# Kernel tuning notes

Measured on AMD Instinct MI355X. Metric: run time of the kernel, lower is better.

## Reference

```python
import jax, jax.numpy as jnp
import numpy as np

B, N, D = 8, 900, 256
SA_H, CA_H = 8, 8
L, P = 4, 4
FF = 2048
SHAPES = ((128, 128), (64, 64), (32, 32), (16, 16))
STARTS = (0, 16384, 20480, 21504)
S = 21760
D_BAND = (D // 6) * 2   # 84
D_ROPE = 3 * D_BAND     # 252
NF = D_BAND // 2        # 42
EPS = 1e-5


def _ln(x, g, b):
    mu = jnp.mean(x, -1, keepdims=True)
    var = jnp.mean((x - mu) ** 2, -1, keepdims=True)
    return (x - mu) * jax.lax.rsqrt(var + EPS) * g + b


def _rotate_half(x):
    x1 = x[..., 0::2]
    x2 = x[..., 1::2]
    return jnp.stack([-x2, x1], axis=-1).reshape(x.shape)


def _rope(q, k, boxes):
    freqs = 1.0 / (10000.0 ** (jnp.arange(NF, dtype=jnp.float32) / NF))
    cx, cy = boxes[..., 0], boxes[..., 1]
    xy = cx * cy

    def cs(v, f):
        a = v[..., None] * f
        return jnp.repeat(jnp.cos(a), 2, -1), jnp.repeat(jnp.sin(a), 2, -1)

    cx_c, cx_s = cs(cx, freqs)
    cy_c, cy_s = cs(cy, freqs)
    xy_c, xy_s = cs(xy, freqs * 0.1)
    cos = jnp.concatenate([cx_c, cy_c, xy_c], -1)
    sin = jnp.concatenate([cx_s, cy_s, xy_s], -1)

    def app(t):
        a, rest = t[..., :D_ROPE], t[..., D_ROPE:]
        return jnp.concatenate([a * cos + _rotate_half(a) * sin, rest], -1)

    return app(q), app(k)


def _bilinear(img, xy):
    # img: (Hl, Wl, C); xy: (M, 2) normalized in [0,1]
    # torch grid_sample semantics: align_corners=False, zero padding
    Hl, Wl, _ = img.shape
    x = xy[:, 0] * Wl - 0.5
    y = xy[:, 1] * Hl - 0.5
    x0 = jnp.floor(x)
    y0 = jnp.floor(y)
    lx = x - x0
    ly = y - y0
    x0i = x0.astype(jnp.int32)
    y0i = y0.astype(jnp.int32)

    def tap(yi, xi):
        valid = (xi >= 0) & (xi < Wl) & (yi >= 0) & (yi < Hl)
        v = img[jnp.clip(yi, 0, Hl - 1), jnp.clip(xi, 0, Wl - 1)]
        return v * valid[:, None].astype(v.dtype)

    return (tap(y0i, x0i) * ((1 - ly) * (1 - lx))[:, None]
            + tap(y0i, x0i + 1) * ((1 - ly) * lx)[:, None]
            + tap(y0i + 1, x0i) * (ly * (1 - lx))[:, None]
            + tap(y0i + 1, x0i + 1) * (ly * lx)[:, None])


def _forward(tgt, memory, query_pos, ref_boxes, reference_points,
             wq, bq, wk, bk, wv, bv, sa_wo, sa_bo, n1_g, n1_b,
             off_w, off_b, aw_w, aw_b, val_w, val_b, co_w, co_b,
             n2_g, n2_b, ff1_w, ff1_b, ff2_w, ff2_b, n3_g, n3_b):
    dh = D // SA_H
    # --- self attention with ComplexRoPE2D applied pre-projection ---
    q = tgt + query_pos
    k = tgt + query_pos
    q, k = _rope(q, k, ref_boxes)
    qh = (q @ wq + bq).reshape(B, N, SA_H, dh).transpose(0, 2, 1, 3)
    kh = (k @ wk + bk).reshape(B, N, SA_H, dh).transpose(0, 2, 1, 3)
    vh = (tgt @ wv + bv).reshape(B, N, SA_H, dh).transpose(0, 2, 1, 3)
    att = jax.nn.softmax(jnp.einsum('bhqd,bhkd->bhqk', qh, kh) * (dh ** -0.5), axis=-1)
    sa = jnp.einsum('bhqk,bhkd->bhqd', att, vh).transpose(0, 2, 1, 3).reshape(B, N, D)
    tgt = _ln(tgt + sa @ sa_wo + sa_bo, n1_g, n1_b)

    # --- multi-scale deformable cross-attention ---
    cdh = D // CA_H
    q2 = tgt + query_pos
    value = (memory @ val_w + val_b).reshape(B, S, CA_H, cdh)
    off = (q2 @ off_w + off_b).reshape(B, N, CA_H, L, P, 2)
    aw = jax.nn.softmax((q2 @ aw_w + aw_b).reshape(B, N, CA_H, L * P), axis=-1)
    aw = aw.reshape(B, N, CA_H, L, P)
    # offset normalizer is (W, H) per level
    normalizer = jnp.array([[w_, h_] for (h_, w_) in SHAPES], dtype=jnp.float32)
    loc = reference_points[:, :, None, :, None, :] + off / normalizer[None, None, None, :, None, :]
    out = jnp.zeros((B, CA_H, N, cdh), dtype=tgt.dtype)
    for l, (Hl, Wl) in enumerate(SHAPES):
        st = STARTS[l]
        v_l = value[:, st:st + Hl * Wl].reshape(B, Hl, Wl, CA_H, cdh)
        v_l = v_l.transpose(0, 3, 1, 2, 4).reshape(B * CA_H, Hl, Wl, cdh)
        loc_l = loc[:, :, :, l].transpose(0, 2, 1, 3, 4).reshape(B * CA_H, N * P, 2)
        s_l = jax.vmap(_bilinear)(v_l, loc_l).reshape(B, CA_H, N, P, cdh)
        out = out + jnp.einsum('bhnpd,bnhp->bhnd', s_l, aw[:, :, :, l])
    ca = out.transpose(0, 2, 1, 3).reshape(B, N, D) @ co_w + co_b
    tgt = _ln(tgt + ca, n2_g, n2_b)

    # --- FFN ---
    ff = jax.nn.relu(tgt @ ff1_w + ff1_b) @ ff2_w + ff2_b
    return _ln(tgt + ff, n3_g, n3_b)


def setup_inputs() -> dict:
    key = jax.random.key(0)
    ks = jax.random.split(key, 16)

    def wmat(k, shape):
        return jax.random.normal(k, shape, jnp.float32) * 0.02

    z = lambda *s: jnp.zeros(s, jnp.float32)
    o = lambda *s: jnp.ones(s, jnp.float32)
    return dict(
        tgt=jax.random.normal(ks[0], (B, N, D), jnp.float32),
        memory=jax.random.normal(ks[1], (B, S, D), jnp.float32),
        query_pos=jax.random.normal(ks[2], (B, N, D), jnp.float32) * 0.02,
        ref_boxes=jax.random.uniform(ks[3], (B, N, 4), jnp.float32),
        reference_points=jax.random.uniform(ks[4], (B, N, L, 2), jnp.float32),
        wq=wmat(ks[5], (D, D)), bq=z(D),
        wk=wmat(ks[6], (D, D)), bk=z(D),
        wv=wmat(ks[7], (D, D)), bv=z(D),
        sa_wo=wmat(ks[8], (D, D)), sa_bo=z(D),
        n1_g=o(D), n1_b=z(D),
        off_w=wmat(ks[9], (D, CA_H * L * P * 2)), off_b=z(CA_H * L * P * 2),
        aw_w=wmat(ks[10], (D, CA_H * L * P)), aw_b=z(CA_H * L * P),
        val_w=wmat(ks[11], (D, D)), val_b=z(D),
        co_w=wmat(ks[12], (D, D)), co_b=z(D),
        n2_g=o(D), n2_b=z(D),
        ff1_w=wmat(ks[13], (D, FF)), ff1_b=z(FF),
        ff2_w=wmat(ks[14], (FF, D)), ff2_b=z(D),
        n3_g=o(D), n3_b=z(D))


def reference(tgt, memory, query_pos, ref_boxes, reference_points,
              wq, bq, wk, bk, wv, bv, sa_wo, sa_bo, n1_g, n1_b,
              off_w, off_b, aw_w, aw_b, val_w, val_b, co_w, co_b,
              n2_g, n2_b, ff1_w, ff1_b, ff2_w, ff2_b, n3_g, n3_b):
    return _forward(tgt, memory, query_pos, ref_boxes, reference_points,
                    wq, bq, wk, bk, wv, bv, sa_wo, sa_bo, n1_g, n1_b,
                    off_w, off_b, aw_w, aw_b, val_w, val_b, co_w, co_b,
                    n2_g, n2_b, ff1_w, ff1_b, ff2_w, ff2_b, n3_g, n3_b)
```

## Files before the change

### kernel.cpp

```cpp
#include <hip/hip_runtime.h>
#include <hip/hip_bf16.h>
#include <math.h>

#define B_ 8
#define N_ 900
#define D_ 256
#define S_ 21760
#define H_ 8
#define DH 32
#define FF_ 2048
#define NROWS (B_*N_)

typedef __attribute__((ext_vector_type(8))) short bf16x8;
typedef __attribute__((ext_vector_type(4))) float f32x4;

union BU { bf16x8 v; short s[8]; unsigned long long u[2]; };

static __device__ inline short f2bf_s(float x) {
  __hip_bfloat16 h = __float2bfloat16(x);
  return *reinterpret_cast<short*>(&h);
}

__device__ __forceinline__ void gload_lds16(const float* g, float* lds) {
  __builtin_amdgcn_global_load_lds(
      (const __attribute__((address_space(1))) void*)g,
      (__attribute__((address_space(3))) void*)lds, 16, 0, 0);
}

__global__ __launch_bounds__(128) void rope_kernel(
    const float* __restrict__ tgt, const float* __restrict__ qpos,
    const float* __restrict__ boxes, __hip_bfloat16* __restrict__ out)
{
  int row = blockIdx.x;
  int tid = threadIdx.x;
  const float* x = tgt  + (size_t)row * D_;
  const float* p = qpos + (size_t)row * D_;
  float a0 = x[2*tid]   + p[2*tid];
  float a1 = x[2*tid+1] + p[2*tid+1];
  float o0 = a0, o1 = a1;
  if (tid < 126) {
    int band = tid / 42;
    int fi   = tid - band * 42;
    float freq = powf(10000.0f, -(float)fi / 42.0f);
    float cx = boxes[(size_t)row*4 + 0];
    float cy = boxes[(size_t)row*4 + 1];
    float v  = (band == 0) ? cx : (band == 1 ? cy : cx * cy);
    if (band == 2) freq *= 0.1f;
    float ang = v * freq;
    float c = cosf(ang), s = sinf(ang);
    o0 = a0 * c - a1 * s;
    o1 = a1 * c + a0 * s;
  }
  short2 sv = make_short2(f2bf_s(o0), f2bf_s(o1));
  *(short2*)&out[(size_t)row*D_ + 2*tid] = sv;
}

__global__ __launch_bounds__(256) void wtrans_kernel(
    const float* __restrict__ wq, const float* __restrict__ wk,
    const float* __restrict__ wv, const float* __restrict__ sa_wo,
    const float* __restrict__ offw, const float* __restrict__ valw,
    const float* __restrict__ cow, const float* __restrict__ aww,
    const float* __restrict__ ff1w, const float* __restrict__ ff2w,
    short* __restrict__ Wt)
{
  int bid = blockIdx.x;
  const float* W; short* out; int K, N, tile;
  if (bid < 448) {
    int wi = bid >> 6; tile = bid & 63; K = 256; N = 256;
    const float* tab[7] = {wq, wk, wv, sa_wo, offw, valw, cow};
    const int   off[7]  = {0, 65536, 131072, 196608, 262144, 360448, 425984};
    W = tab[wi]; out = Wt + off[wi];
  } else if (bid < 480) {
    tile = bid - 448; K = 256; N = 128; W = aww; out = Wt + 327680;
  } else if (bid < 992) {
    tile = bid - 480; K = 256; N = 2048; W = ff1w; out = Wt + 491520;
  } else {
    tile = bid - 992; K = 2048; N = 256; W = ff2w; out = Wt + 1015808;
  }
  int ntn = N >> 5;
  int tk = tile / ntn, tn = tile - tk * ntn;
  __shared__ float t[32][33];
  int c = threadIdx.x & 31, rr = threadIdx.x >> 5;
  #pragma unroll
  for (int i = 0; i < 4; ++i)
    t[rr + i*8][c] = W[(size_t)(tk*32 + rr + i*8) * N + tn*32 + c];
  __syncthreads();
  #pragma unroll
  for (int i = 0; i < 4; ++i)
    out[(size_t)(tn*32 + rr + i*8) * K + tk*32 + c] = f2bf_s(t[c][rr + i*8]);
}

template<int BM, int KK, bool ABF16, bool A2ADD, bool RELU, int OUTMODE, int AUX>
__global__ __launch_bounds__(256) void mgemm_kernel(
    const void* __restrict__ Ap, const float* __restrict__ A2p,
    const short* __restrict__ Wt,
    const float* __restrict__ bias, const float* __restrict__ bias2,
    void* __restrict__ Cp, void* __restrict__ Cp2, int M, int N,
    const float* __restrict__ Xres, const float* __restrict__ lng,
    const float* __restrict__ lnb)
{
  constexpr int MS = BM / 16;
  constexpr bool SWAP = (OUTMODE != 2);
  __shared__ short As[BM * 256];
  int tid = threadIdx.x;
  int w = tid >> 6, lane = tid & 63;
  int g = lane >> 4, r = lane & 15;
  int m0 = blockIdx.x * BM;
  int nw = blockIdx.y * 256 + w * 64;
  bool active = nw < N;

  f32x4 acc[MS][4];
  #pragma unroll
  for (int i = 0; i < MS; ++i)
    #pragma unroll
    for (int j = 0; j < 4; ++j) acc[i][j] = (f32x4){0.f,0.f,0.f,0.f};

  for (int kb = 0; kb < KK; kb += 256) {
    if (KK > 256 && kb) __syncthreads();
    #pragma unroll
    for (int i = 0; i < BM/8; ++i) {
      int u = i*256 + tid;
      int row = u >> 5, c8 = u & 31;
      BU pk;
      if (ABF16) {
        pk.v = *(const bf16x8*)((const short*)Ap + (size_t)(m0+row)*KK + kb + c8*8);
      } else {
        const float* ap = (const float*)Ap + (size_t)(m0+row)*KK + kb + c8*8;
        float4 a0 = *(const float4*)ap;
        float4 a1 = *(const float4*)(ap + 4);
        if (A2ADD) {
          const float* a2 = A2p + (size_t)(m0+row)*KK + kb + c8*8;
          float4 b0 = *(const float4*)a2;
          float4 b1 = *(const float4*)(a2 + 4);
          a0.x += b0.x; a0.y += b0.y; a0.z += b0.z; a0.w += b0.w;
          a1.x += b1.x; a1.y += b1.y; a1.z += b1.z; a1.w += b1.w;
        }
        pk.s[0]=f2bf_s(a0.x); pk.s[1]=f2bf_s(a0.y); pk.s[2]=f2bf_s(a0.z); pk.s[3]=f2bf_s(a0.w);
        pk.s[4]=f2bf_s(a1.x); pk.s[5]=f2bf_s(a1.y); pk.s[6]=f2bf_s(a1.z); pk.s[7]=f2bf_s(a1.w);
      }
      int col = (c8*8) ^ ((row & 7) << 3);
      *(bf16x8*)&As[row*256 + col] = pk.v;
    }
    __syncthreads();
    if (active) {
      #pragma unroll
      for (int kk = 0; kk < 8; ++kk) {
        BU bfr[4];
        #pragma unroll
        for (int ns = 0; ns < 4; ++ns) {
          const short* wp = Wt + (size_t)(nw + ns*16 + r)*KK + kb + kk*32;
          bfr[ns].u[0] = *(const unsigned long long*)(wp + 4*g);
          bfr[ns].u[1] = *(const unsigned long long*)(wp + 16 + 4*g);
        }
        #pragma unroll
        for (int ms = 0; ms < MS; ++ms) {
          int row = ms*16 + r;
          int c0 = (kk*32 + g*4)      ^ ((r & 7) << 3);
          int c1 = (kk*32 + 16 + g*4) ^ ((r & 7) << 3);
          BU af;
          af.u[0] = *(const unsigned long long*)&As[row*256 + c0];
          af.u[1] = *(const unsigned long long*)&As[row*256 + c1];
          #pragma unroll
          for (int ns = 0; ns < 4; ++ns) {
            if (SWAP)
              acc[ms][ns] = __builtin_amdgcn_mfma_f32_16x16x32_bf16(
                  bfr[ns].v, af.v, acc[ms][ns], 0, 0, 0);
            else
              acc[ms][ns] = __builtin_amdgcn_mfma_f32_16x16x32_bf16(
                  af.v, bfr[ns].v, acc[ms][ns], 0, 0, 0);
          }
        }
      }
    }
  }

  if (OUTMODE == 5) {
    float vv[MS][16];
    float ps[MS], pq[MS];
    #pragma unroll
    for (int ms = 0; ms < MS; ++ms) {
      ps[ms] = 0.f; pq[ms] = 0.f;
      int m = m0 + ms*16 + r;
      #pragma unroll
      for (int ns = 0; ns < 4; ++ns) {
        int n0 = nw + ns*16 + g*4;
        float4 b4 = *(const float4*)&bias[n0];
        float4 x4 = *(const float4*)&Xres[(size_t)m*256 + n0];
        #pragma unroll
        for (int j = 0; j < 4; ++j) {
          float v = acc[ms][ns][j] + ((const float*)&b4)[j] + ((const float*)&x4)[j];
          vv[ms][ns*4 + j] = v;
          ps[ms] += v; pq[ms] += v*v;
        }
      }
      ps[ms] += __shfl_xor(ps[ms], 16); ps[ms] += __shfl_xor(ps[ms], 32);
      pq[ms] += __shfl_xor(pq[ms], 16); pq[ms] += __shfl_xor(pq[ms], 32);
    }
    __syncthreads();
    float* red = (float*)As;
    if (g == 0) {
      #pragma unroll
      for (int ms = 0; ms < MS; ++ms) {
        red[(ms*16 + r)*8 + w]     = ps[ms];
        red[(ms*16 + r)*8 + 4 + w] = pq[ms];
      }
    }
    __syncthreads();
    #pragma unroll
    for (int ms = 0; ms < MS; ++ms) {
      int rowi = ms*16 + r;
      float ts = red[rowi*8+0]+red[rowi*8+1]+red[rowi*8+2]+red[rowi*8+3];
      float tq = red[rowi*8+4]+red[rowi*8+5]+red[rowi*8+6]+red[rowi*8+7];
      float mu = ts * (1.0f/256.0f);
      float var = tq * (1.0f/256.0f) - mu*mu;
      float rs = rsqrtf(fmaxf(var, 0.f) + 1e-5f);
      int m = m0 + ms*16 + r;
      #pragma unroll
      for (int ns = 0; ns < 4; ++ns) {
        int n0 = nw + ns*16 + g*4;
        float4 g4 = *(const float4*)&lng[n0];
        float4 be = *(const float4*)&lnb[n0];
        float4 ov;
        ov.x = (vv[ms][ns*4+0] - mu)*rs*g4.x + be.x;
        ov.y = (vv[ms][ns*4+1] - mu)*rs*g4.y + be.y;
        ov.z = (vv[ms][ns*4+2] - mu)*rs*g4.z + be.z;
        ov.w = (vv[ms][ns*4+3] - mu)*rs*g4.w + be.w;
        *(float4*)&((float*)Cp)[(size_t)m*256 + n0] = ov;
        if (AUX == 1) {
          float4 q4 = *(const float4*)&A2p[(size_t)m*256 + n0];
          short4 sv = make_short4(
              f2bf_s(ov.x + q4.x), f2bf_s(ov.y + q4.y),
              f2bf_s(ov.z + q4.z), f2bf_s(ov.w + q4.w));
          *(short4*)&((short*)Cp2)[(size_t)m*256 + n0] = sv;
        } else if (AUX == 2) {
          short4 sv = make_short4(
              f2bf_s(ov.x), f2bf_s(ov.y), f2bf_s(ov.z), f2bf_s(ov.w));
          *(short4*)&((short*)Cp2)[(size_t)m*256 + n0] = sv;
        }
      }
    }
    return;
  }

  if (!active) return;

  #pragma unroll
  for (int ms = 0; ms < MS; ++ms) {
    #pragma unroll
    for (int ns = 0; ns < 4; ++ns) {
      if (SWAP) {
        int n0 = nw + ns*16 + g*4;
        int m  = m0 + ms*16 + r;
        float4 b4;
        if (OUTMODE == 3 || OUTMODE == 4)
          b4 = (n0 < 256) ? *(const float4*)&bias[n0]
                          : *(const float4*)&bias2[n0 - 256];
        else
          b4 = *(const float4*)&bias[n0];
        float v0 = acc[ms][ns][0] + b4.x;
        float v1 = acc[ms][ns][1] + b4.y;
        float v2 = acc[ms][ns][2] + b4.z;
        float v3 = acc[ms][ns][3] + b4.w;
        if (RELU) {
          v0 = fmaxf(v0, 0.f); v1 = fmaxf(v1, 0.f);
          v2 = fmaxf(v2, 0.f); v3 = fmaxf(v3, 0.f);
        }
        if (OUTMODE == 0) {
          *(float4*)&((float*)Cp)[(size_t)m*N + n0] = make_float4(v0,v1,v2,v3);
        } else if (OUTMODE == 1) {
          short4 sv = make_short4(f2bf_s(v0), f2bf_s(v1), f2bf_s(v2), f2bf_s(v3));
          *(short4*)&((short*)Cp)[(size_t)m*N + n0] = sv;
        } else if (OUTMODE == 3) {
          short4 sv = make_short4(f2bf_s(v0), f2bf_s(v1), f2bf_s(v2), f2bf_s(v3));
          if (n0 < 256) *(short4*)&((short*)Cp )[(size_t)m*256 + n0]       = sv;
          else          *(short4*)&((short*)Cp2)[(size_t)m*256 + (n0-256)] = sv;
        } else {
          float4 fv = make_float4(v0,v1,v2,v3);
          if (n0 < 256) *(float4*)&((float*)Cp )[(size_t)m*256 + n0]       = fv;
          else          *(float4*)&((float*)Cp2)[(size_t)m*128 + (n0-256)] = fv;
        }
      } else {
        int n = nw + ns*16 + r;
        float bsc = bias[n];
        int hh = n >> 5, dd = n & 31;
        int mb = m0 + ms*16 + g*4;
        short4 sv = make_short4(
            f2bf_s(acc[ms][ns][0] + bsc), f2bf_s(acc[ms][ns][1] + bsc),
            f2bf_s(acc[ms][ns][2] + bsc), f2bf_s(acc[ms][ns][3] + bsc));
        int bb = mb / N_, bbe = (mb + 3) / N_;
        if (bb == bbe) {
          int nn = mb - bb * N_;
          *(short4*)&((short*)Cp)[((size_t)((bb*H_ + hh)*DH + dd))*N_ + nn] = sv;
        } else {
          const short* sp = (const short*)&sv;
          #pragma unroll
          for (int j = 0; j < 4; ++j) {
            int m = mb + j;
            int b2 = m / N_, nn = m - b2 * N_;
            ((short*)Cp)[((size_t)((b2*H_ + hh)*DH + dd))*N_ + nn] = sp[j];
          }
        }
      }
    }
  }
}

__global__ __launch_bounds__(512) void vgemm_kernel(
    const float* __restrict__ Ap, const short* __restrict__ Wt,
    const float* __restrict__ bias, short* __restrict__ Cp)
{
  __shared__ float buf[8][1024];
  __shared__ float dump[1024];
  int tid = threadIdx.x;
  int w = tid >> 6, l = tid & 63;
  int g = l >> 4, r = l & 15;
  int nw = w * 32;

  BU wreg[2][8];
  #pragma unroll
  for (int ns = 0; ns < 2; ++ns) {
    const short* wp = Wt + (size_t)(nw + ns*16 + r) * 256;
    #pragma unroll
    for (int kk = 0; kk < 8; ++kk) {
      wreg[ns][kk].u[0] = *(const unsigned long long*)(wp + kk*32 + 4*g);
      wreg[ns][kk].u[1] = *(const unsigned long long*)(wp + kk*32 + 16 + 4*g);
    }
  }
  float4 bs4[2];
  #pragma unroll
  for (int ns = 0; ns < 2; ++ns) bs4[ns] = *(const float4*)&bias[nw + ns*16 + g*4];

  bool stager = (w < 4);
  int srow = (w & 3)*8 + (l >> 3);
  int schunk = (l & 7) ^ (srow & 7);
  const float* gbase = Ap + ((size_t)blockIdx.x*160 + srow) * 256 + schunk*4;

  if (stager) {
    #pragma unroll
    for (int t = 0; t < 4; ++t)
      gload_lds16(gbase + (t>>3)*8192 + (t&7)*32, &buf[t][(w & 3)*256]);
  }

  f32x4 acc[2][2];
  #pragma unroll
  for (int i = 0; i < 2; ++i)
    #pragma unroll
    for (int j = 0; j < 2; ++j) acc[i][j] = (f32x4){0.f,0.f,0.f,0.f};

  int bb = blockIdx.x / 136;
  int pixblk = (blockIdx.x % 136) * 160;

  for (int s = 0; s < 5; ++s) {
    #pragma unroll
    for (int cp = 0; cp < 4; ++cp) {
      int c = cp*2;
      int t = s*8 + c;
      if (stager) {
        int tn0 = t + 4, tn1 = t + 5;
        if (tn0 < 40) gload_lds16(gbase + (tn0>>3)*8192 + (tn0&7)*32,
                                  &buf[(c+4)&7][(w & 3)*256]);
        else          gload_lds16(gbase, &dump[(w & 3)*256]);
        if (tn1 < 40) gload_lds16(gbase + (tn1>>3)*8192 + (tn1&7)*32,
                                  &buf[(c+5)&7][(w & 3)*256]);
        else          gload_lds16(gbase, &dump[(w & 3)*256]);
        asm volatile("s_waitcnt vmcnt(4)" ::: "memory");
      }
      __builtin_amdgcn_s_barrier();
      #pragma unroll
      for (int cc = 0; cc < 2; ++cc) {
        int ci = c + cc;
        const float* bp = &buf[ci][0];
        #pragma unroll
        for (int ms = 0; ms < 2; ++ms) {
          int row = ms*16 + r;
          const float* rp = bp + row*32;
          float4 f0 = *(const float4*)&rp[((g    ) ^ (row & 7)) * 4];
          float4 f1 = *(const float4*)&rp[((g + 4) ^ (row & 7)) * 4];
          BU af;
          af.s[0]=f2bf_s(f0.x); af.s[1]=f2bf_s(f0.y); af.s[2]=f2bf_s(f0.z); af.s[3]=f2bf_s(f0.w);
          af.s[4]=f2bf_s(f1.x); af.s[5]=f2bf_s(f1.y); af.s[6]=f2bf_s(f1.z); af.s[7]=f2bf_s(f1.w);
          #pragma unroll
          for (int ns = 0; ns < 2; ++ns)
            acc[ms][ns] = __builtin_amdgcn_mfma_f32_16x16x32_bf16(
                wreg[ns][ci].v, af.v, acc[ms][ns], 0, 0, 0);
        }
      }
    }
    int pix0 = pixblk + s*32;
    #pragma unroll
    for (int ms = 0; ms < 2; ++ms) {
      #pragma unroll
      for (int ns = 0; ns < 2; ++ns) {
        int pix = pix0 + ms*16 + r;
        int n0  = nw + ns*16 + g*4;
        int hh = n0 >> 5, dd = n0 & 31;
        short4 sv = make_short4(
            f2bf_s(acc[ms][ns][0] + bs4[ns].x),
            f2bf_s(acc[ms][ns][1] + bs4[ns].y),
            f2bf_s(acc[ms][ns][2] + bs4[ns].z),
            f2bf_s(acc[ms][ns][3] + bs4[ns].w));
        *(short4*)&Cp[((size_t)(bb*H_ + hh)*S_ + pix)*32 + dd] = sv;
        acc[ms][ns] = (f32x4){0.f,0.f,0.f,0.f};
      }
    }
  }
}

__global__ __launch_bounds__(64) void mfma_attn_kernel(
    const __hip_bfloat16* __restrict__ Q,
    const __hip_bfloat16* __restrict__ K,
    const __hip_bfloat16* __restrict__ Vt,
    __hip_bfloat16* __restrict__ O)
{
  const int NQT = 29;
  int wid = blockIdx.x;
  int qt = wid % NQT, bh = wid / NQT;
  int b = bh >> 3, h = bh & 7;
  int lane = threadIdx.x;
  int g = lane >> 4, r = lane & 15;
  int q0 = qt * 32;
  const float scale = 0.17677669529663687f;

  union U { bf16x8 v; short s[8]; unsigned long long u64[2]; };

  U qf[2];
  #pragma unroll
  for (int qq = 0; qq < 2; ++qq) {
    int qrow = min(q0 + qq*16 + r, N_ - 1);
    const __hip_bfloat16* qp = Q + ((size_t)(b*N_ + qrow))*D_ + h*DH;
    qf[qq].u64[0] = *(const unsigned long long*)(qp + 4*g);
    qf[qq].u64[1] = *(const unsigned long long*)(qp + 16 + 4*g);
  }

  f32x4 oaccA[2], oaccB[2];
  #pragma unroll
  for (int qq = 0; qq < 2; ++qq) {
    oaccA[qq] = (f32x4){0.f,0.f,0.f,0.f};
    oaccB[qq] = (f32x4){0.f,0.f,0.f,0.f};
  }
  float m0v = -1e30f, m1v = -1e30f, l0v = 0.f, l1v = 0.f;
  const f32x4 zero = {0.f,0.f,0.f,0.f};

  const __hip_bfloat16* vbase0 = Vt + (size_t)(bh*DH + r) * N_;
  const __hip_bfloat16* vbase1 = Vt + (size_t)(bh*DH + 16 + r) * N_;

  for (int kt = 0; kt < N_; kt += 32) {
    U kf0, kf1;
    {
      int kr0 = min(kt + r, N_ - 1);
      int kr1 = min(kt + 16 + r, N_ - 1);
      const __hip_bfloat16* kp0 = K + ((size_t)(b*N_ + kr0))*D_ + h*DH;
      const __hip_bfloat16* kp1 = K + ((size_t)(b*N_ + kr1))*D_ + h*DH;
      kf0.u64[0] = *(const unsigned long long*)(kp0 + 4*g);
      kf0.u64[1] = *(const unsigned long long*)(kp0 + 16 + 4*g);
      kf1.u64[0] = *(const unsigned long long*)(kp1 + 4*g);
      kf1.u64[1] = *(const unsigned long long*)(kp1 + 16 + 4*g);
    }
    U vf0, vf1;
    vf0.u64[0] = *(const unsigned long long*)(vbase0 + kt + 4*g);
    vf0.u64[1] = *(const unsigned long long*)(vbase0 + kt + 16 + 4*g);
    vf1.u64[0] = *(const unsigned long long*)(vbase1 + kt + 4*g);
    vf1.u64[1] = *(const unsigned long long*)(vbase1 + kt + 16 + 4*g);

    #pragma unroll
    for (int qq = 0; qq < 2; ++qq) {
      f32x4 s0 = __builtin_amdgcn_mfma_f32_16x16x32_bf16(kf0.v, qf[qq].v, zero, 0, 0, 0);
      f32x4 s1 = __builtin_amdgcn_mfma_f32_16x16x32_bf16(kf1.v, qf[qq].v, zero, 0, 0, 0);
      float m = qq ? m1v : m0v;
      float lv = qq ? l1v : l0v;

      float sc[8];
      #pragma unroll
      for (int j = 0; j < 4; ++j) {
        sc[j]   = (kt + 4*g + j      < N_) ? s0[j] * scale : -1e30f;
        sc[4+j] = (kt + 16 + 4*g + j < N_) ? s1[j] * scale : -1e30f;
      }
      float mx = sc[0];
      #pragma unroll
      for (int j = 1; j < 8; ++j) mx = fmaxf(mx, sc[j]);
      mx = fmaxf(mx, __shfl_xor(mx, 16));
      mx = fmaxf(mx, __shfl_xor(mx, 32));

      float mnew = fmaxf(m, mx);
      float corr = __expf(m - mnew);
      float p[8], ps = 0.f;
      #pragma unroll
      for (int j = 0; j < 8; ++j) { p[j] = __expf(sc[j] - mnew); ps += p[j]; }
      ps += __shfl_xor(ps, 16);
      ps += __shfl_xor(ps, 32);
      lv = lv * corr + ps;
      if (qq) { m1v = mnew; l1v = lv; } else { m0v = mnew; l0v = lv; }
      #pragma unroll
      for (int j = 0; j < 4; ++j) { oaccA[qq][j] *= corr; oaccB[qq][j] *= corr; }

      U pf;
      #pragma unroll
      for (int j = 0; j < 8; ++j) pf.s[j] = f2bf_s(p[j]);

      oaccA[qq] = __builtin_amdgcn_mfma_f32_16x16x32_bf16(vf0.v, pf.v, oaccA[qq], 0, 0, 0);
      oaccB[qq] = __builtin_amdgcn_mfma_f32_16x16x32_bf16(vf1.v, pf.v, oaccB[qq], 0, 0, 0);
    }
  }

  #pragma unroll
  for (int qq = 0; qq < 2; ++qq) {
    int qrow = q0 + qq*16 + r;
    if (qrow < N_) {
      float inv = 1.0f / (qq ? l1v : l0v);
      short* op = (short*)(O + ((size_t)(b*N_ + qrow))*D_ + h*DH);
      short4 sA = make_short4(
          f2bf_s(oaccA[qq][0]*inv), f2bf_s(oaccA[qq][1]*inv),
          f2bf_s(oaccA[qq][2]*inv), f2bf_s(oaccA[qq][3]*inv));
      short4 sB = make_short4(
          f2bf_s(oaccB[qq][0]*inv), f2bf_s(oaccB[qq][1]*inv),
          f2bf_s(oaccB[qq][2]*inv), f2bf_s(oaccB[qq][3]*inv));
      *(short4*)&op[4*g]      = sA;
      *(short4*)&op[16 + 4*g] = sB;
    }
  }
}

__global__ __launch_bounds__(256) void sample4_kernel(
    const __hip_bfloat16* __restrict__ V, const float* __restrict__ offp,
    const float* __restrict__ awl, const float* __restrict__ refp,
    short* __restrict__ out)
{
  int tid = threadIdx.x;
  int q = tid >> 6, t = tid & 63;
  int row = blockIdx.x * 4 + q;
  int b = row / N_;
  __shared__ float s_aw[4][128];
  __shared__ float s_loc[4][256];
  #pragma unroll
  for (int i = 0; i < 2; ++i)
    s_aw[q][t + i*64] = awl[(size_t)row*128 + t + i*64];
  {
    const float norms[4] = {128.f, 64.f, 32.f, 16.f};
    #pragma unroll
    for (int i = 0; i < 4; ++i) {
      int e = t + i*64;
      int rem = e & 31, li = rem >> 3, ax = rem & 1;
      s_loc[q][e] = refp[((size_t)row*4 + li)*2 + ax]
                  + offp[(size_t)row*256 + e] / norms[li];
    }
  }
  __syncthreads();
  if (t < 8) {
    float mx = -1e30f;
    for (int j = 0; j < 16; ++j) mx = fmaxf(mx, s_aw[q][t*16+j]);
    float sum = 0.f;
    for (int j = 0; j < 16; ++j) sum += __expf(s_aw[q][t*16+j] - mx);
    float inv = 1.0f / sum;
    for (int j = 0; j < 16; ++j)
      s_aw[q][t*16+j] = __expf(s_aw[q][t*16+j] - mx) * inv;
  }
  __syncthreads();
  int h = t >> 3, dq = t & 7;
  const int dims[4]   = {128, 64, 32, 16};
  const int starts[4] = {0, 16384, 20480, 21504};
  const __hip_bfloat16* Vb = V + ((size_t)(b*H_ + h) * S_) * 32 + dq*4;
  float a0 = 0.f, a1 = 0.f, a2 = 0.f, a3 = 0.f;
  #pragma unroll
  for (int l = 0; l < 4; ++l) {
    int Wl = dims[l], st = starts[l];
    #pragma unroll
    for (int p = 0; p < 4; ++p) {
      float lx = s_loc[q][h*32 + l*8 + p*2 + 0];
      float ly = s_loc[q][h*32 + l*8 + p*2 + 1];
      float x = lx * Wl - 0.5f, y = ly * Wl - 0.5f;
      float x0f = floorf(x), y0f = floorf(y);
      float fx = x - x0f, fy = y - y0f;
      int x0 = (int)x0f, y0 = (int)y0f;
      float v0 = 0.f, v1 = 0.f, v2 = 0.f, v3 = 0.f;
      #pragma unroll
      for (int ty = 0; ty < 2; ++ty) {
        int yi = y0 + ty;
        float wy = ty ? fy : (1.f - fy);
        if (yi < 0 || yi >= Wl) continue;
        #pragma unroll
        for (int txi = 0; txi < 2; ++txi) {
          int xi = x0 + txi;
          float wx = txi ? fx : (1.f - fx);
          if (xi < 0 || xi >= Wl) continue;
          unsigned long long vv =
              *(const unsigned long long*)&Vb[(size_t)(st + yi*Wl + xi) * 32];
          float ww = wy * wx;
          v0 += ww * __uint_as_float((unsigned)(vv) << 16);
          v1 += ww * __uint_as_float((unsigned)(vv) & 0xffff0000u);
          v2 += ww * __uint_as_float((unsigned)(vv >> 32) << 16);
          v3 += ww * __uint_as_float((unsigned)(vv >> 32) & 0xffff0000u);
        }
      }
      float aw = s_aw[q][h*16 + l*4 + p];
      a0 += aw * v0; a1 += aw * v1; a2 += aw * v2; a3 += aw * v3;
    }
  }
  short4 sv = make_short4(f2bf_s(a0), f2bf_s(a1), f2bf_s(a2), f2bf_s(a3));
  *(short4*)&out[(size_t)row*D_ + h*DH + dq*4] = sv;
}

extern "C" void kernel_launch(void* const* d_in, const int* in_sizes, int n_in,
                              void* d_out, int out_size, void* d_ws, size_t ws_size,
                              hipStream_t stream)
{
  const float* tgt    = (const float*)d_in[0];
  const float* memory = (const float*)d_in[1];
  const float* qpos   = (const float*)d_in[2];
  const float* boxes  = (const float*)d_in[3];
  const float* refp   = (const float*)d_in[4];
  const float* wq = (const float*)d_in[5];   const float* bq = (const float*)d_in[6];
  const float* wk = (const float*)d_in[7];   const float* bk = (const float*)d_in[8];
  const float* wv = (const float*)d_in[9];   const float* bv = (const float*)d_in[10];
  const float* sa_wo = (const float*)d_in[11]; const float* sa_bo = (const float*)d_in[12];
  const float* n1g = (const float*)d_in[13]; const float* n1b = (const float*)d_in[14];
  const float* off_w = (const float*)d_in[15]; const float* off_b = (const float*)d_in[16];
  const float* aw_w  = (const float*)d_in[17]; const float* aw_b  = (const float*)d_in[18];
  const float* val_w = (const float*)d_in[19]; const float* val_b = (const float*)d_in[20];
  const float* co_w  = (const float*)d_in[21]; const float* co_b  = (const float*)d_in[22];
  const float* n2g = (const float*)d_in[23]; const float* n2b = (const float*)d_in[24];
  const float* ff1_w = (const float*)d_in[25]; const float* ff1_b = (const float*)d_in[26];
  const float* ff2_w = (const float*)d_in[27]; const float* ff2_b = (const float*)d_in[28];
  const float* n3g = (const float*)d_in[29]; const float* n3b = (const float*)d_in[30];

  char* ws = (char*)d_ws;
  size_t NE = (size_t)NROWS * D_;
  __hip_bfloat16* Vv = (__hip_bfloat16*)ws;
  __hip_bfloat16* FFM = (__hip_bfloat16*)ws;
  size_t p = (size_t)B_ * S_ * D_ * sizeof(__hip_bfloat16);
  float* A  = (float*)(ws + p); p += NE*4;
  float* Qb = (float*)(ws + p); p += NE*4;
  float* Kb = (float*)(ws + p); p += NE*4;
  float* Vh = (float*)(ws + p); p += NE*4;
  float* S1 = (float*)(ws + p); p += NE*4;
  float* S2 = (float*)(ws + p); p += NE*4;
  float* T1 = (float*)(ws + p); p += NE*4;
  short* Wt = (short*)((char*)Kb + NE*2);
  float* out = (float*)d_out;
  (void)ws_size; (void)in_sizes; (void)n_in; (void)out_size;

  const short* qk_t  = Wt;
  const short* wv_t  = Wt + 131072;
  const short* sa_t  = Wt + 196608;
  const short* offaw_t = Wt + 262144;
  const short* val_t = Wt + 360448;
  const short* co_t  = Wt + 425984;
  const short* ff1_t = Wt + 491520;
  const short* ff2_t = Wt + 1015808;

  wtrans_kernel<<<1504, 256, 0, stream>>>(wq, wk, wv, sa_wo, off_w, val_w,
                                          co_w, aw_w, ff1_w, ff2_w, Wt);

  rope_kernel<<<NROWS, 128, 0, stream>>>(tgt, qpos, boxes, (__hip_bfloat16*)A);
  mgemm_kernel<32,256,true,false,false,3,0><<<dim3(225,2), 256, 0, stream>>>(
      A, nullptr, qk_t, bq, bk, Qb, Kb, NROWS, 512, nullptr, nullptr, nullptr);
  mgemm_kernel<32,256,false,false,false,2,0><<<dim3(225,1), 256, 0, stream>>>(
      tgt, nullptr, wv_t, bv, nullptr, Vh, nullptr, NROWS, 256, nullptr, nullptr, nullptr);
  mfma_attn_kernel<<<29 * B_ * H_, 64, 0, stream>>>(
      (const __hip_bfloat16*)Qb, (const __hip_bfloat16*)Kb,
      (const __hip_bfloat16*)Vh, (__hip_bfloat16*)S1);
  mgemm_kernel<32,256,true,false,false,5,1><<<dim3(225,1), 256, 0, stream>>>(
      S1, qpos, sa_t, sa_bo, nullptr, T1, S2, NROWS, 256, tgt, n1g, n1b);

  vgemm_kernel<<<1088, 512, 0, stream>>>(memory, val_t, val_b, (short*)Vv);
  mgemm_kernel<32,256,true,false,false,4,0><<<dim3(225,2), 256, 0, stream>>>(
      S2, nullptr, offaw_t, off_b, aw_b, Qb, Kb, NROWS, 384, nullptr, nullptr, nullptr);
  sample4_kernel<<<NROWS/4, 256, 0, stream>>>(Vv, Qb, Kb, refp, (short*)S1);
  mgemm_kernel<32,256,true,false,false,5,2><<<dim3(225,1), 256, 0, stream>>>(
      S1, nullptr, co_t, co_b, nullptr, T1, S2, NROWS, 256, T1, n2g, n2b);

  mgemm_kernel<64,256,true,false,true,1,0><<<dim3(113,8), 256, 0, stream>>>(
      S2, nullptr, ff1_t, ff1_b, nullptr, FFM, nullptr, NROWS, FF_, nullptr, nullptr, nullptr);
  mgemm_kernel<32,2048,true,false,false,5,0><<<dim3(225,1), 256, 0, stream>>>(
      FFM, nullptr, ff2_t, ff2_b, nullptr, out, nullptr, NROWS, 256, T1, n3g, n3b);
}
```

Before: 389.8 us.

## Merge attention into value-projection GEMM launch as extra blocks for concurrency

The self-attention kernel is folded into the memory value-projection GEMM launch. Blocks past 1088 each run eight independent attention waves, so the two independent stages share one grid and can overlap on the GPU. This removes one launch and fills the GPU better, since the attention alone had only 1856 single-wave blocks. The risk is that attention waves now sit in 512-thread blocks that reserve the GEMM's large shared-memory allocation, which can lower occupancy for the attention work.

```diff
diff --git a/kernel.cpp b/kernel.cpp
--- a/kernel.cpp
+++ b/kernel.cpp
@@ -305,14 +305,134 @@
   }
 }
 
-__global__ __launch_bounds__(512) void vgemm_kernel(
+__device__ __forceinline__ void attn_wave_body(
+    int wid, int lane,
+    const __hip_bfloat16* __restrict__ Q,
+    const __hip_bfloat16* __restrict__ K,
+    const __hip_bfloat16* __restrict__ Vt,
+    __hip_bfloat16* __restrict__ O)
+{
+  const int NQT = 29;
+  int qt = wid % NQT, bh = wid / NQT;
+  int b = bh >> 3, h = bh & 7;
+  int g = lane >> 4, r = lane & 15;
+  int q0 = qt * 32;
+  const float scale = 0.17677669529663687f;
+
+  BU qf[2];
+  #pragma unroll
+  for (int qq = 0; qq < 2; ++qq) {
+    int qrow = min(q0 + qq*16 + r, N_ - 1);
+    const __hip_bfloat16* qp = Q + ((size_t)(b*N_ + qrow))*D_ + h*DH;
+    qf[qq].u[0] = *(const unsigned long long*)(qp + 4*g);
+    qf[qq].u[1] = *(const unsigned long long*)(qp + 16 + 4*g);
+  }
+
+  f32x4 oaccA[2], oaccB[2];
+  #pragma unroll
+  for (int qq = 0; qq < 2; ++qq) {
+    oaccA[qq] = (f32x4){0.f,0.f,0.f,0.f};
+    oaccB[qq] = (f32x4){0.f,0.f,0.f,0.f};
+  }
+  float m0v = -1e30f, m1v = -1e30f, l0v = 0.f, l1v = 0.f;
+  const f32x4 zero = {0.f,0.f,0.f,0.f};
+
+  const __hip_bfloat16* vbase0 = Vt + (size_t)(bh*DH + r) * N_;
+  const __hip_bfloat16* vbase1 = Vt + (size_t)(bh*DH + 16 + r) * N_;
+
+  for (int kt = 0; kt < N_; kt += 32) {
+    BU kf0, kf1;
+    {
+      int kr0 = min(kt + r, N_ - 1);
+      int kr1 = min(kt + 16 + r, N_ - 1);
+      const __hip_bfloat16* kp0 = K + ((size_t)(b*N_ + kr0))*D_ + h*DH;
+      const __hip_bfloat16* kp1 = K + ((size_t)(b*N_ + kr1))*D_ + h*DH;
+      kf0.u[0] = *(const unsigned long long*)(kp0 + 4*g);
+      kf0.u[1] = *(const unsigned long long*)(kp0 + 16 + 4*g);
+      kf1.u[0] = *(const unsigned long long*)(kp1 + 4*g);
+      kf1.u[1] = *(const unsigned long long*)(kp1 + 16 + 4*g);
+    }
+    BU vf0, vf1;
+    vf0.u[0] = *(const unsigned long long*)(vbase0 + kt + 4*g);
+    vf0.u[1] = *(const unsigned long long*)(vbase0 + kt + 16 + 4*g);
+    vf1.u[0] = *(const unsigned long long*)(vbase1 + kt + 4*g);
+    vf1.u[1] = *(const unsigned long long*)(vbase1 + kt + 16 + 4*g);
+
+    #pragma unroll
+    for (int qq = 0; qq < 2; ++qq) {
+      f32x4 s0 = __builtin_amdgcn_mfma_f32_16x16x32_bf16(kf0.v, qf[qq].v, zero, 0, 0, 0);
+      f32x4 s1 = __builtin_amdgcn_mfma_f32_16x16x32_bf16(kf1.v, qf[qq].v, zero, 0, 0, 0);
+      float m = qq ? m1v : m0v;
+      float lv = qq ? l1v : l0v;
+
+      float sc[8];
+      #pragma unroll
+      for (int j = 0; j < 4; ++j) {
+        sc[j]   = (kt + 4*g + j      < N_) ? s0[j] * scale : -1e30f;
+        sc[4+j] = (kt + 16 + 4*g + j < N_) ? s1[j] * scale : -1e30f;
+      }
+      float mx = sc[0];
+      #pragma unroll
+      for (int j = 1; j < 8; ++j) mx = fmaxf(mx, sc[j]);
+      mx = fmaxf(mx, __shfl_xor(mx, 16));
+      mx = fmaxf(mx, __shfl_xor(mx, 32));
+
+      float mnew = fmaxf(m, mx);
+      float corr = __expf(m - mnew);
+      float p[8], ps = 0.f;
+      #pragma unroll
+      for (int j = 0; j < 8; ++j) { p[j] = __expf(sc[j] - mnew); ps += p[j]; }
+      ps += __shfl_xor(ps, 16);
+      ps += __shfl_xor(ps, 32);
+      lv = lv * corr + ps;
+      if (qq) { m1v = mnew; l1v = lv; } else { m0v = mnew; l0v = lv; }
+      #pragma unroll
+      for (int j = 0; j < 4; ++j) { oaccA[qq][j] *= corr; oaccB[qq][j] *= corr; }
+
+      BU pf;
+      #pragma unroll
+      for (int j = 0; j < 8; ++j) pf.s[j] = f2bf_s(p[j]);
+
+      oaccA[qq] = __builtin_amdgcn_mfma_f32_16x16x32_bf16(vf0.v, pf.v, oaccA[qq], 0, 0, 0);
+      oaccB[qq] = __builtin_amdgcn_mfma_f32_16x16x32_bf16(vf1.v, pf.v, oaccB[qq], 0, 0, 0);
+    }
+  }
+
+  #pragma unroll
+  for (int qq = 0; qq < 2; ++qq) {
+    int qrow = q0 + qq*16 + r;
+    if (qrow < N_) {
+      float inv = 1.0f / (qq ? l1v : l0v);
+      short* op = (short*)(O + ((size_t)(b*N_ + qrow))*D_ + h*DH);
+      short4 sA = make_short4(
+          f2bf_s(oaccA[qq][0]*inv), f2bf_s(oaccA[qq][1]*inv),
+          f2bf_s(oaccA[qq][2]*inv), f2bf_s(oaccA[qq][3]*inv));
+      short4 sB = make_short4(
+          f2bf_s(oaccB[qq][0]*inv), f2bf_s(oaccB[qq][1]*inv),
+          f2bf_s(oaccB[qq][2]*inv), f2bf_s(oaccB[qq][3]*inv));
+      *(short4*)&op[4*g]      = sA;
+      *(short4*)&op[16 + 4*g] = sB;
+    }
+  }
+}
+
+__global__ __launch_bounds__(512) void vgemm_attn_kernel(
     const float* __restrict__ Ap, const short* __restrict__ Wt,
-    const float* __restrict__ bias, short* __restrict__ Cp)
+    const float* __restrict__ bias, short* __restrict__ Cp,
+    const __hip_bfloat16* __restrict__ Q, const __hip_bfloat16* __restrict__ K,
+    const __hip_bfloat16* __restrict__ Vt, __hip_bfloat16* __restrict__ O)
 {
   __shared__ float buf[8][1024];
   __shared__ float dump[1024];
   int tid = threadIdx.x;
   int w = tid >> 6, l = tid & 63;
+
+  if (blockIdx.x >= 1088) {
+    int unit = (blockIdx.x - 1088) * 8 + w;
+    attn_wave_body(unit, l, Q, K, Vt, O);
+    return;
+  }
+
   int g = l >> 4, r = l & 15;
   int nw = w * 32;
 
@@ -402,120 +522,6 @@
         *(short4*)&Cp[((size_t)(bb*H_ + hh)*S_ + pix)*32 + dd] = sv;
         acc[ms][ns] = (f32x4){0.f,0.f,0.f,0.f};
       }
-    }
-  }
-}
-
-__global__ __launch_bounds__(64) void mfma_attn_kernel(
-    const __hip_bfloat16* __restrict__ Q,
-    const __hip_bfloat16* __restrict__ K,
-    const __hip_bfloat16* __restrict__ Vt,
-    __hip_bfloat16* __restrict__ O)
-{
-  const int NQT = 29;
-  int wid = blockIdx.x;
-  int qt = wid % NQT, bh = wid / NQT;
-  int b = bh >> 3, h = bh & 7;
-  int lane = threadIdx.x;
-  int g = lane >> 4, r = lane & 15;
-  int q0 = qt * 32;
-  const float scale = 0.17677669529663687f;
-
-  union U { bf16x8 v; short s[8]; unsigned long long u64[2]; };
-
-  U qf[2];
-  #pragma unroll
-  for (int qq = 0; qq < 2; ++qq) {
-    int qrow = min(q0 + qq*16 + r, N_ - 1);
-    const __hip_bfloat16* qp = Q + ((size_t)(b*N_ + qrow))*D_ + h*DH;
-    qf[qq].u64[0] = *(const unsigned long long*)(qp + 4*g);
-    qf[qq].u64[1] = *(const unsigned long long*)(qp + 16 + 4*g);
-  }
-
-  f32x4 oaccA[2], oaccB[2];
-  #pragma unroll
-  for (int qq = 0; qq < 2; ++qq) {
-    oaccA[qq] = (f32x4){0.f,0.f,0.f,0.f};
-    oaccB[qq] = (f32x4){0.f,0.f,0.f,0.f};
-  }
-  float m0v = -1e30f, m1v = -1e30f, l0v = 0.f, l1v = 0.f;
-  const f32x4 zero = {0.f,0.f,0.f,0.f};
-
-  const __hip_bfloat16* vbase0 = Vt + (size_t)(bh*DH + r) * N_;
-  const __hip_bfloat16* vbase1 = Vt + (size_t)(bh*DH + 16 + r) * N_;
-
-  for (int kt = 0; kt < N_; kt += 32) {
-    U kf0, kf1;
-    {
-      int kr0 = min(kt + r, N_ - 1);
-      int kr1 = min(kt + 16 + r, N_ - 1);
-      const __hip_bfloat16* kp0 = K + ((size_t)(b*N_ + kr0))*D_ + h*DH;
-      const __hip_bfloat16* kp1 = K + ((size_t)(b*N_ + kr1))*D_ + h*DH;
-      kf0.u64[0] = *(const unsigned long long*)(kp0 + 4*g);
-      kf0.u64[1] = *(const unsigned long long*)(kp0 + 16 + 4*g);
-      kf1.u64[0] = *(const unsigned long long*)(kp1 + 4*g);
-      kf1.u64[1] = *(const unsigned long long*)(kp1 + 16 + 4*g);
-    }
-    U vf0, vf1;
-    vf0.u64[0] = *(const unsigned long long*)(vbase0 + kt + 4*g);
-    vf0.u64[1] = *(const unsigned long long*)(vbase0 + kt + 16 + 4*g);
-    vf1.u64[0] = *(const unsigned long long*)(vbase1 + kt + 4*g);
-    vf1.u64[1] = *(const unsigned long long*)(vbase1 + kt + 16 + 4*g);
-
-    #pragma unroll
-    for (int qq = 0; qq < 2; ++qq) {
-      f32x4 s0 = __builtin_amdgcn_mfma_f32_16x16x32_bf16(kf0.v, qf[qq].v, zero, 0, 0, 0);
-      f32x4 s1 = __builtin_amdgcn_mfma_f32_16x16x32_bf16(kf1.v, qf[qq].v, zero, 0, 0, 0);
-      float m = qq ? m1v : m0v;
-      float lv = qq ? l1v : l0v;
-
-      float sc[8];
-      #pragma unroll
-      for (int j = 0; j < 4; ++j) {
-        sc[j]   = (kt + 4*g + j      < N_) ? s0[j] * scale : -1e30f;
-        sc[4+j] = (kt + 16 + 4*g + j < N_) ? s1[j] * scale : -1e30f;
-      }
-      float mx = sc[0];
-      #pragma unroll
-      for (int j = 1; j < 8; ++j) mx = fmaxf(mx, sc[j]);
-      mx = fmaxf(mx, __shfl_xor(mx, 16));
-      mx = fmaxf(mx, __shfl_xor(mx, 32));
-
-      float mnew = fmaxf(m, mx);
-      float corr = __expf(m - mnew);
-      float p[8], ps = 0.f;
-      #pragma unroll
-      for (int j = 0; j < 8; ++j) { p[j] = __expf(sc[j] - mnew); ps += p[j]; }
-      ps += __shfl_xor(ps, 16);
-      ps += __shfl_xor(ps, 32);
-      lv = lv * corr + ps;
-      if (qq) { m1v = mnew; l1v = lv; } else { m0v = mnew; l0v = lv; }
-      #pragma unroll
-      for (int j = 0; j < 4; ++j) { oaccA[qq][j] *= corr; oaccB[qq][j] *= corr; }
-
-      U pf;
-      #pragma unroll
-      for (int j = 0; j < 8; ++j) pf.s[j] = f2bf_s(p[j]);
-
-      oaccA[qq] = __builtin_amdgcn_mfma_f32_16x16x32_bf16(vf0.v, pf.v, oaccA[qq], 0, 0, 0);
-      oaccB[qq] = __builtin_amdgcn_mfma_f32_16x16x32_bf16(vf1.v, pf.v, oaccB[qq], 0, 0, 0);
-    }
-  }
-
-  #pragma unroll
-  for (int qq = 0; qq < 2; ++qq) {
-    int qrow = q0 + qq*16 + r;
-    if (qrow < N_) {
-      float inv = 1.0f / (qq ? l1v : l0v);
-      short* op = (short*)(O + ((size_t)(b*N_ + qrow))*D_ + h*DH);
-      short4 sA = make_short4(
-          f2bf_s(oaccA[qq][0]*inv), f2bf_s(oaccA[qq][1]*inv),
-          f2bf_s(oaccA[qq][2]*inv), f2bf_s(oaccA[qq][3]*inv));
-      short4 sB = make_short4(
-          f2bf_s(oaccB[qq][0]*inv), f2bf_s(oaccB[qq][1]*inv),
-          f2bf_s(oaccB[qq][2]*inv), f2bf_s(oaccB[qq][3]*inv));
-      *(short4*)&op[4*g]      = sA;
-      *(short4*)&op[16 + 4*g] = sB;
     }
   }
 }
@@ -655,13 +661,15 @@
       A, nullptr, qk_t, bq, bk, Qb, Kb, NROWS, 512, nullptr, nullptr, nullptr);
   mgemm_kernel<32,256,false,false,false,2,0><<<dim3(225,1), 256, 0, stream>>>(
       tgt, nullptr, wv_t, bv, nullptr, Vh, nullptr, NROWS, 256, nullptr, nullptr, nullptr);
-  mfma_attn_kernel<<<29 * B_ * H_, 64, 0, stream>>>(
+
+  vgemm_attn_kernel<<<1320, 512, 0, stream>>>(
+      memory, val_t, val_b, (short*)Vv,
       (const __hip_bfloat16*)Qb, (const __hip_bfloat16*)Kb,
       (const __hip_bfloat16*)Vh, (__hip_bfloat16*)S1);
+
   mgemm_kernel<32,256,true,false,false,5,1><<<dim3(225,1), 256, 0, stream>>>(
       S1, qpos, sa_t, sa_bo, nullptr, T1, S2, NROWS, 256, tgt, n1g, n1b);
 
-  vgemm_kernel<<<1088, 512, 0, stream>>>(memory, val_t, val_b, (short*)Vv);
   mgemm_kernel<32,256,true,false,false,4,0><<<dim3(225,2), 256, 0, stream>>>(
       S2, nullptr, offaw_t, off_b, aw_b, Qb, Kb, NROWS, 384, nullptr, nullptr, nullptr);
   sample4_kernel<<<NROWS/4, 256, 0, stream>>>(Vv, Qb, Kb, refp, (short*)S1);
```

Measured after the change: 394.4 us. Within noise of the previous version (+1.2%).
